# Optimization experiments

Measured on AMD Instinct MI355X. Metric: run time of the kernel, lower is better.

Reference implementation:

```python
import jax, jax.numpy as jnp
import numpy as np

B, L, D, M, R, W = 4, 2048, 2048, 64, 128, 4
SCALE = 1.0 / float(np.sqrt(M))
NORM_EPS = 1e-12


def setup_inputs() -> dict:
    key = jax.random.key(0)
    ks = jax.random.split(key, 8)
    s = lambda k, shape: jax.random.normal(k, shape, jnp.float32) * 0.02
    return dict(
        hidden_states=jax.random.normal(ks[0], (B, L, D), jnp.float32),
        conv_w=s(ks[1], (D, W)),                 # depthwise conv kernel (squeezed [D,1,W])
        conv_b=jnp.zeros((D,), jnp.float32),
        in_proj_w=s(ks[2], (2 * M, D)),          # r,k projection
        ch_gate_w0=s(ks[3], (R, D)),             # low-rank channel gate
        ch_gate_w1=s(ks[4], (D, R)),
        ch_gate_b1=jnp.zeros((D,), jnp.float32),
        mem_gate_w=s(ks[5], (2 * M, D)),         # select/tau gates
        mem_gate_b=jax.random.normal(ks[6], (2 * M,), jnp.float32),
        residual_weight=jnp.ones((D,), jnp.float32),
    )


def _causal_depthwise_conv(x, w, b):
    # x: [B,L,D], w: [D,W], b: [D]; y[t] = sum_i x[t-(W-1)+i] * w[:, i] + b
    xp = jnp.pad(x, ((0, 0), (W - 1, 0), (0, 0)))
    y = sum(xp[:, i:i + x.shape[1], :] * w[:, i] for i in range(W)) + b
    return jax.nn.silu(y)


def reference(hidden_states, conv_w, conv_b, in_proj_w, ch_gate_w0, ch_gate_w1,
              ch_gate_b1, mem_gate_w, mem_gate_b, residual_weight):
    x = hidden_states
    shift = _causal_depthwise_conv(x, conv_w, conv_b)          # [B,L,D]
    residual = shift

    rk = shift @ in_proj_w.T                                   # [B,L,2M]
    r, k = rk[..., :M], rk[..., M:]

    ch = jax.nn.sigmoid((x @ ch_gate_w0.T) @ ch_gate_w1.T + ch_gate_b1)
    u = ch * x                                                 # [B,L,D] gated value

    mg = shift @ mem_gate_w.T + mem_gate_b                     # [B,L,2M]
    sel = jax.nn.softplus(mg[..., :M])
    tau = jax.nn.sigmoid(mg[..., M:])
    it_gate = sel ** tau                                       # input gate
    g = -sel * tau                                             # log decay (rt_gate_log)

    # F.normalize(k) then scale by input gate
    k = k / jnp.maximum(jnp.linalg.norm(k, axis=-1, keepdims=True), NORM_EPS)
    k = k * it_gate

    # GLA recurrence: S_t = diag(exp(g_t)) S_{t-1} + k_t^T u_t; o_t = scale * r_t S_t
    def step(S, inp):
        r_t, k_t, u_t, g_t = inp                               # [B,M],[B,M],[B,D],[B,M]
        S = jnp.exp(g_t)[..., None] * S + k_t[..., None] * u_t[:, None, :]
        o_t = SCALE * jnp.einsum('bm,bmd->bd', r_t, S)
        return S, o_t

    xs = (jnp.swapaxes(r, 0, 1), jnp.swapaxes(k, 0, 1),
          jnp.swapaxes(u, 0, 1), jnp.swapaxes(g, 0, 1))
    S0 = jnp.zeros((x.shape[0], M, D), jnp.float32)
    _, o = jax.lax.scan(step, S0, xs)                          # o: [L,B,D]
    o = jnp.swapaxes(o, 0, 1)

    return o + residual * residual_weight
```

## Files before the change

kernel.cpp:

```cpp
#include <hip/hip_runtime.h>
#include <hip/hip_bf16.h>
#include <math.h>

#define B_ 4
#define L_ 2048
#define D_ 2048
#define M_ 64
#define R_ 128
#define NTOK (B_*L_)
#define SCALE_ 0.125f
#define C_ 32
#define NCH (L_/C_)

typedef __attribute__((ext_vector_type(8))) short short8;
typedef __attribute__((ext_vector_type(4))) float f32x4;

#define BAR() asm volatile("s_waitcnt lgkmcnt(0)\n\ts_barrier" ::: "memory")

#define MFMA(a, b, c) __builtin_amdgcn_mfma_f32_16x16x32_bf16((a), (b), (c), 0, 0, 0)

__device__ __forceinline__ unsigned short f2bfu(float v) {
    union { float f; unsigned u; } a; a.f = v;
    unsigned r = a.u + 0x7fffu + ((a.u >> 16) & 1u);
    return (unsigned short)(r >> 16);
}
__device__ __forceinline__ float bfu2f(unsigned short h) {
    union { unsigned u; float f; } a; a.u = ((unsigned)h) << 16;
    return a.f;
}
__device__ __forceinline__ unsigned pkbf(float a, float b) {
    union { __hip_bfloat162 h; unsigned u; } cv;
    cv.h = __float22bfloat162_rn(make_float2(a, b));
    return cv.u;
}

__global__ __launch_bounds__(256) void k_conv(const float* __restrict__ x,
    const float* __restrict__ cw, const float* __restrict__ cb,
    float* __restrict__ shift, unsigned short* __restrict__ sbf,
    unsigned short* __restrict__ xb)
{
    size_t i4 = (size_t)blockIdx.x * 256 + threadIdx.x;
    int dq = (int)(i4 % (D_ / 4));
    size_t n = i4 / (D_ / 4);
    int l = (int)(n % L_);
    int d0 = dq * 4;
    const float* xp = x + n * D_ + d0;
    float4 w0 = *(const float4*)(cw + (size_t)d0 * 4);
    float4 w1 = *(const float4*)(cw + (size_t)(d0 + 1) * 4);
    float4 w2 = *(const float4*)(cw + (size_t)(d0 + 2) * 4);
    float4 w3 = *(const float4*)(cw + (size_t)(d0 + 3) * 4);
    float4 acc = *(const float4*)(cb + d0);
    float4 xv3 = *(const float4*)xp;
#pragma unroll
    for (int i = 0; i < 3; i++) {
        if (l - 3 + i >= 0) {
            float4 xv = *(const float4*)(xp + (size_t)(i - 3) * D_);
            acc.x = fmaf(xv.x, ((const float*)&w0)[i], acc.x);
            acc.y = fmaf(xv.y, ((const float*)&w1)[i], acc.y);
            acc.z = fmaf(xv.z, ((const float*)&w2)[i], acc.z);
            acc.w = fmaf(xv.w, ((const float*)&w3)[i], acc.w);
        }
    }
    acc.x = fmaf(xv3.x, ((const float*)&w0)[3], acc.x);
    acc.y = fmaf(xv3.y, ((const float*)&w1)[3], acc.y);
    acc.z = fmaf(xv3.z, ((const float*)&w2)[3], acc.z);
    acc.w = fmaf(xv3.w, ((const float*)&w3)[3], acc.w);
    float4 o;
    o.x = acc.x / (1.f + expf(-acc.x));
    o.y = acc.y / (1.f + expf(-acc.y));
    o.z = acc.z / (1.f + expf(-acc.z));
    o.w = acc.w / (1.f + expf(-acc.w));
    *(float4*)(shift + n * D_ + d0) = o;
    uint2 sp; sp.x = pkbf(o.x, o.y); sp.y = pkbf(o.z, o.w);
    *(uint2*)(sbf + n * D_ + d0) = sp;
    uint2 xpk; xpk.x = pkbf(xv3.x, xv3.y); xpk.y = pkbf(xv3.z, xv3.w);
    *(uint2*)(xb + n * D_ + d0) = xpk;
}

__global__ __launch_bounds__(256) void k_castw(
    const float* __restrict__ s0, const float* __restrict__ s1,
    const float* __restrict__ s2, const float* __restrict__ s3,
    unsigned short* __restrict__ d0, unsigned short* __restrict__ d1,
    unsigned short* __restrict__ d2, unsigned short* __restrict__ d3)
{
    int which = blockIdx.x >> 8;
    int idx = ((blockIdx.x & 255) * 256 + threadIdx.x) * 4;
    const float* s = which == 0 ? s0 : which == 1 ? s1 : which == 2 ? s2 : s3;
    unsigned short* d = which == 0 ? d0 : which == 1 ? d1 : which == 2 ? d2 : d3;
    float4 v = *(const float4*)(s + idx);
    uint2 o;
    o.x = pkbf(v.x, v.y);
    o.y = pkbf(v.z, v.w);
    *(uint2*)(d + idx) = o;
}

__global__ __launch_bounds__(256) void k_gemm12(
    const unsigned short* __restrict__ sbf, const unsigned short* __restrict__ xb,
    const unsigned short* __restrict__ Wcatb, const unsigned short* __restrict__ w0b,
    float* __restrict__ rkmg, unsigned short* __restrict__ t1b)
{
    __shared__ __align__(16) unsigned short As[2][128 * 32];
    __shared__ __align__(16) unsigned short Bs[2][128 * 32];
    int tid = threadIdx.x;
    int n0 = blockIdx.x * 128;
    int y = blockIdx.y;
    const unsigned short* A = (y < 2) ? sbf : xb;
    const unsigned short* Bp = (y == 0) ? Wcatb : (y == 1) ? (Wcatb + 128 * 2048) : w0b;
    int wave = tid >> 6, lane = tid & 63;
    int quad = lane >> 4, lcol = lane & 15;
    int wrow = (wave >> 1) * 64, wcol = (wave & 1) * 64;
    int r0 = tid >> 2;
    int sub = (tid & 3) * 8;
    const unsigned short* a0p = A + (size_t)(n0 + r0) * 2048 + sub;
    const unsigned short* a1p = A + (size_t)(n0 + r0 + 64) * 2048 + sub;
    const unsigned short* b0p = Bp + (size_t)r0 * 2048 + sub;
    const unsigned short* b1p = Bp + (size_t)(r0 + 64) * 2048 + sub;

    f32x4 acc[4][4];
#pragma unroll
    for (int i = 0; i < 4; i++)
#pragma unroll
        for (int j = 0; j < 4; j++) acc[i][j] = {0.f, 0.f, 0.f, 0.f};

    uint4 av0 = *(const uint4*)a0p, av1 = *(const uint4*)a1p;
    uint4 bv0 = *(const uint4*)b0p, bv1 = *(const uint4*)b1p;
    {
        int i0 = tid * 8, i1 = 2048 + tid * 8;
        *(uint4*)&As[0][i0] = av0; *(uint4*)&As[0][i1] = av1;
        *(uint4*)&Bs[0][i0] = bv0; *(uint4*)&Bs[0][i1] = bv1;
    }
    av0 = *(const uint4*)(a0p + 32); av1 = *(const uint4*)(a1p + 32);
    bv0 = *(const uint4*)(b0p + 32); bv1 = *(const uint4*)(b1p + 32);
    BAR();

    for (int k32 = 0; k32 < 64; k32++) {
        int cur = k32 & 1;
        short8 af[4], bfr[4];
#pragma unroll
        for (int i = 0; i < 4; i++)
            af[i] = *(short8*)&As[cur][(wrow + i * 16 + lcol) * 32 + quad * 8];
#pragma unroll
        for (int j = 0; j < 4; j++)
            bfr[j] = *(short8*)&Bs[cur][(wcol + j * 16 + lcol) * 32 + quad * 8];
#pragma unroll
        for (int i = 0; i < 4; i++)
#pragma unroll
            for (int j = 0; j < 4; j++)
                acc[i][j] = MFMA(af[i], bfr[j], acc[i][j]);
        if (k32 + 1 < 64) {
            int nb = cur ^ 1;
            int i0 = tid * 8, i1 = 2048 + tid * 8;
            *(uint4*)&As[nb][i0] = av0; *(uint4*)&As[nb][i1] = av1;
            *(uint4*)&Bs[nb][i0] = bv0; *(uint4*)&Bs[nb][i1] = bv1;
        }
        if (k32 + 2 < 64) {
            int k0 = (k32 + 2) * 32;
            av0 = *(const uint4*)(a0p + k0); av1 = *(const uint4*)(a1p + k0);
            bv0 = *(const uint4*)(b0p + k0); bv1 = *(const uint4*)(b1p + k0);
        }
        BAR();
    }

#pragma unroll
    for (int i = 0; i < 4; i++)
#pragma unroll
        for (int j = 0; j < 4; j++)
#pragma unroll
            for (int q = 0; q < 4; q++) {
                int row = wrow + i * 16 + quad * 4 + q;
                int col = wcol + j * 16 + lcol;
                int n = n0 + row;
                if (y < 2) rkmg[(size_t)n * 256 + y * 128 + col] = acc[i][j][q];
                else       t1b[(size_t)n * 128 + col] = f2bfu(acc[i][j][q]);
            }
}

__global__ __launch_bounds__(256) void k_gemm3(
    const unsigned short* __restrict__ t1b, const unsigned short* __restrict__ w1b,
    const float* __restrict__ b1, const float* __restrict__ x,
    float* __restrict__ u)
{
    __shared__ __align__(16) unsigned short As[2][128 * 32];
    __shared__ __align__(16) unsigned short Bs[2][128 * 32];
    int tid = threadIdx.x;
    int n0 = blockIdx.x * 128;
    int jblk = blockIdx.y * 128;
    int wave = tid >> 6, lane = tid & 63;
    int quad = lane >> 4, lcol = lane & 15;
    int wrow = (wave >> 1) * 64, wcol = (wave & 1) * 64;
    int r0 = tid >> 2;
    int sub = (tid & 3) * 8;
    const unsigned short* a0p = t1b + (size_t)(n0 + r0) * 128 + sub;
    const unsigned short* a1p = t1b + (size_t)(n0 + r0 + 64) * 128 + sub;
    const unsigned short* b0p = w1b + (size_t)(jblk + r0) * 128 + sub;
    const unsigned short* b1p = w1b + (size_t)(jblk + r0 + 64) * 128 + sub;

    f32x4 acc[4][4];
#pragma unroll
    for (int i = 0; i < 4; i++)
#pragma unroll
        for (int j = 0; j < 4; j++) acc[i][j] = {0.f, 0.f, 0.f, 0.f};

    uint4 av0 = *(const uint4*)a0p, av1 = *(const uint4*)a1p;
    uint4 bv0 = *(const uint4*)b0p, bv1 = *(const uint4*)b1p;
    {
        int i0 = tid * 8, i1 = 2048 + tid * 8;
        *(uint4*)&As[0][i0] = av0; *(uint4*)&As[0][i1] = av1;
        *(uint4*)&Bs[0][i0] = bv0; *(uint4*)&Bs[0][i1] = bv1;
    }
    av0 = *(const uint4*)(a0p + 32); av1 = *(const uint4*)(a1p + 32);
    bv0 = *(const uint4*)(b0p + 32); bv1 = *(const uint4*)(b1p + 32);
    BAR();

    for (int k32 = 0; k32 < 4; k32++) {
        int cur = k32 & 1;
        short8 af[4], bfr[4];
#pragma unroll
        for (int i = 0; i < 4; i++)
            af[i] = *(short8*)&As[cur][(wrow + i * 16 + lcol) * 32 + quad * 8];
#pragma unroll
        for (int j = 0; j < 4; j++)
            bfr[j] = *(short8*)&Bs[cur][(wcol + j * 16 + lcol) * 32 + quad * 8];
#pragma unroll
        for (int i = 0; i < 4; i++)
#pragma unroll
            for (int j = 0; j < 4; j++)
                acc[i][j] = MFMA(af[i], bfr[j], acc[i][j]);
        if (k32 + 1 < 4) {
            int nb = cur ^ 1;
            int i0 = tid * 8, i1 = 2048 + tid * 8;
            *(uint4*)&As[nb][i0] = av0; *(uint4*)&As[nb][i1] = av1;
            *(uint4*)&Bs[nb][i0] = bv0; *(uint4*)&Bs[nb][i1] = bv1;
        }
        if (k32 + 2 < 4) {
            int k0 = (k32 + 2) * 32;
            av0 = *(const uint4*)(a0p + k0); av1 = *(const uint4*)(a1p + k0);
            bv0 = *(const uint4*)(b0p + k0); bv1 = *(const uint4*)(b1p + k0);
        }
        BAR();
    }

#pragma unroll
    for (int i = 0; i < 4; i++)
#pragma unroll
        for (int j = 0; j < 4; j++)
#pragma unroll
            for (int q = 0; q < 4; q++) {
                int row = wrow + i * 16 + quad * 4 + q;
                int col = wcol + j * 16 + lcol;
                int n = n0 + row, jc = jblk + col;
                float val = acc[i][j][q] + b1[jc];
                val = 1.f / (1.f + expf(-val));
                val *= x[(size_t)n * D_ + jc];
                u[(size_t)n * D_ + jc] = val;
            }
}

__global__ __launch_bounds__(256) void k_prep(const float* __restrict__ rkmg,
    const float* __restrict__ mb,
    unsigned short* __restrict__ Rt, unsigned short* __restrict__ Kc,
    float* __restrict__ Ac, unsigned short* __restrict__ Pg)
{
    __shared__ float seg[4 * 64];
    __shared__ __align__(16) unsigned short rtL[32 * 72];
    __shared__ __align__(16) unsigned short kdL[32 * 72];
    int blk = blockIdx.x;
    int sg = threadIdx.x >> 6, mm = threadIdx.x & 63;
    int n0 = blk * C_ + sg * 8;

    float rr[8], kk[8], lamr[8];
    float csum = 0.f;
#pragma unroll
    for (int j = 0; j < 8; j++) {
        const float* row = rkmg + (size_t)(n0 + j) * 256;
        float r   = row[mm];
        float k   = row[64 + mm];
        float mg1 = row[128 + mm] + mb[mm];
        float mg2 = row[192 + mm] + mb[64 + mm];
        float sel = (mg1 > 20.f) ? mg1 : log1pf(expf(mg1));
        float tau = 1.f / (1.f + expf(-mg2));
        float it  = expf(tau * logf(sel));
        float g   = -sel * tau;
        float s2  = k * k;
#pragma unroll
        for (int off = 32; off >= 1; off >>= 1) s2 += __shfl_xor(s2, off, 64);
        float kn = k / fmaxf(sqrtf(s2), 1e-12f);
        rr[j] = r;
        kk[j] = kn * it;
        csum += g;
        lamr[j] = csum;
    }
    seg[sg * 64 + mm] = csum;
    __syncthreads();
    float off = 0.f, tot = 0.f;
#pragma unroll
    for (int s = 0; s < 4; s++) {
        float v = seg[s * 64 + mm];
        if (s < sg) off += v;
        tot += v;
    }
    size_t obase = (size_t)blk * (C_ * 64);
    unsigned short kcp[8];
#pragma unroll
    for (int j = 0; j < 8; j++) {
        float lam = off + lamr[j];
        unsigned short rv = f2bfu(rr[j] * expf(lam));
        unsigned short kv = f2bfu(kk[j] * expf(-lam));
        int t = sg * 8 + j;
        Rt[obase + (size_t)t * 64 + mm] = rv;
        rtL[t * 72 + mm] = rv;
        kdL[t * 72 + mm] = kv;
        kcp[j] = f2bfu(kk[j] * expf(tot - lam));
    }
    ushort4 ka4, kb4;
    ka4.x = kcp[0]; ka4.y = kcp[1]; ka4.z = kcp[2]; ka4.w = kcp[3];
    kb4.x = kcp[4]; kb4.y = kcp[5]; kb4.z = kcp[6]; kb4.w = kcp[7];
    *(ushort4*)&Kc[obase + (size_t)mm * C_ + sg * 8]     = ka4;
    *(ushort4*)&Kc[obase + (size_t)mm * C_ + sg * 8 + 4] = kb4;
    if (sg == 0) Ac[(size_t)blk * 64 + mm] = expf(tot);
    __syncthreads();

    int lane = threadIdx.x & 63, quad = lane >> 4, l15 = lane & 15;
    size_t pb = (size_t)blk * 1024;
    if (sg < 3) {
        int ti = (sg == 0) ? 0 : 16;
        int si = (sg == 2) ? 16 : 0;
        short8 a0 = *(const short8*)&rtL[(ti + l15) * 72 + quad * 8];
        short8 a1 = *(const short8*)&rtL[(ti + l15) * 72 + 32 + quad * 8];
        short8 b0 = *(const short8*)&kdL[(si + l15) * 72 + quad * 8];
        short8 b1 = *(const short8*)&kdL[(si + l15) * 72 + 32 + quad * 8];
        f32x4 pp = {0.f, 0.f, 0.f, 0.f};
        pp = MFMA(a0, b0, pp);
        pp = MFMA(a1, b1, pp);
#pragma unroll
        for (int q = 0; q < 4; q++) {
            int t = ti + quad * 4 + q, s = si + l15;
            Pg[pb + t * 32 + s] = f2bfu((s <= t) ? pp[q] : 0.f);
        }
    } else {
#pragma unroll
        for (int q = 0; q < 4; q++)
            Pg[pb + (quad * 4 + q) * 32 + 16 + l15] = 0;
    }
}

#define STAGE(q) do { \
    int t_ = tid >> 3, m8_ = (tid & 7) * 8; \
    *(uint4*)&rtS[q][t_ * 72 + m8_] = rtv; \
    int m_ = tid >> 2, s8_ = (tid & 3) * 8; \
    *(uint4*)&kcS[q][m_ * 40 + s8_] = kcv; \
    int s4_ = (tid & 7) * 4; \
    *(ushort4*)&PlS[q][t_ * 40 + s4_] = plv; \
    int dd_ = tid & 31, tt_ = tid >> 5; \
    _Pragma("unroll") \
    for (int j_ = 0; j_ < 4; j_++) { \
        unsigned short h_ = f2bfu(uv[j_]); \
        UTh[q][dd_ * 40 + tt_ + 8 * j_] = h_; \
        UTl[q][dd_ * 40 + tt_ + 8 * j_] = f2bfu(uv[j_] - bfu2f(h_)); \
    } \
    if (tid < 64) aCs[q][tid] = acv; \
} while (0)

#define PREFETCH(n) do { \
    size_t g_ = cbase + (size_t)(n) * 2048 + (size_t)tid * 8; \
    rtv = *(const uint4*)(Rt + g_); \
    kcv = *(const uint4*)(Kc + g_); \
    plv = *(const ushort4*)(Pg + pbase + (size_t)(n) * 1024 + tid * 4); \
    size_t un_ = ubase + (size_t)(n) * C_ * D_; \
    int dd_ = tid & 31, tt_ = tid >> 5; \
    _Pragma("unroll") \
    for (int j_ = 0; j_ < 4; j_++) \
        uv[j_] = u[un_ + (size_t)(tt_ + 8 * j_) * D_ + dd_]; \
    if (tid < 64) acv = Ac[(size_t)(bNCH + (n)) * 64 + tid]; \
} while (0)

__global__ __launch_bounds__(256) void k_chunk(
    const unsigned short* __restrict__ Rt, const unsigned short* __restrict__ Kc,
    const float* __restrict__ Ac, const unsigned short* __restrict__ Pg,
    const float* __restrict__ u, const float* __restrict__ shift,
    const float* __restrict__ rw, float* __restrict__ out)
{
    __shared__ __align__(16) unsigned short rtS[2][32 * 72];
    __shared__ __align__(16) unsigned short PlS[2][32 * 40];
    __shared__ __align__(16) unsigned short kcS[2][64 * 40];
    __shared__ __align__(16) unsigned short UTh[2][32 * 40];
    __shared__ __align__(16) unsigned short UTl[2][32 * 40];
    __shared__ __align__(16) unsigned short STh[2][32 * 72];
    __shared__ __align__(16) unsigned short STl[2][32 * 72];
    __shared__ float aCs[2][64];

    int tid = threadIdx.x;
    int wave = tid >> 6, lane = tid & 63;
    int quad = lane >> 4, l15 = lane & 15;
    int b = blockIdx.x & 3, slice = blockIdx.x >> 2;
    int d0 = slice * 32;
    int bNCH = b * NCH;

    for (int i = tid; i < 2 * 32 * 72; i += 256) {
        (&STh[0][0])[i] = 0; (&STl[0][0])[i] = 0;
    }

    size_t cbase = (size_t)b * (L_ * 64);
    size_t pbase = (size_t)bNCH * 1024;
    size_t ubase = (size_t)b * L_ * D_ + d0;

    float rwv = (wave < 2) ? rw[d0 + wave * 16 + l15] : 0.f;

    uint4 rtv, kcv;
    ushort4 plv;
    float uv[4], acv = 0.f;
    float sv[8], svn[8];
    size_t sadr = ubase + (size_t)wave * 16 + l15 + (size_t)(quad * 4) * D_;

    PREFETCH(0);
    STAGE(0);
    PREFETCH(1);
    if (wave < 2) {
#pragma unroll
        for (int tile = 0; tile < 2; tile++)
#pragma unroll
            for (int q = 0; q < 4; q++)
                sv[tile * 4 + q] = shift[sadr + (size_t)(tile * 16 + q) * D_];
    }
    BAR();

    f32x4 zz = {0.f, 0.f, 0.f, 0.f};
    f32x4 sreg[4];
#pragma unroll
    for (int mt = 0; mt < 4; mt++) sreg[mt] = zz;

    for (int c = 0; c < NCH; c++) {
        int p = c & 1;
        if (c + 1 < NCH) STAGE(p ^ 1);
        if (c + 2 < NCH) PREFETCH(c + 2);

        if (wave < 2) {
            if (c + 1 < NCH) {
                size_t s0_ = sadr + (size_t)(c + 1) * C_ * D_;
#pragma unroll
                for (int tile = 0; tile < 2; tile++)
#pragma unroll
                    for (int q = 0; q < 4; q++)
                        svn[tile * 4 + q] = shift[s0_ + (size_t)(tile * 16 + q) * D_];
            }
            int h = wave;
            short8 a00 = *(const short8*)&rtS[p][l15 * 72 + quad * 8];
            short8 a01 = *(const short8*)&rtS[p][l15 * 72 + 32 + quad * 8];
            short8 a10 = *(const short8*)&rtS[p][(16 + l15) * 72 + quad * 8];
            short8 a11 = *(const short8*)&rtS[p][(16 + l15) * 72 + 32 + quad * 8];
            const unsigned short* sbh = &STh[p ^ 1][(h * 16 + l15) * 72];
            const unsigned short* sbl = &STl[p ^ 1][(h * 16 + l15) * 72];
            short8 sh0 = *(const short8*)&sbh[quad * 8];
            short8 sh1 = *(const short8*)&sbh[32 + quad * 8];
            short8 sl0 = *(const short8*)&sbl[quad * 8];
            short8 sl1 = *(const short8*)&sbl[32 + quad * 8];
            short8 pa0 = *(const short8*)&PlS[p][l15 * 40 + quad * 8];
            short8 pa1 = *(const short8*)&PlS[p][(16 + l15) * 40 + quad * 8];
            short8 uh = *(const short8*)&UTh[p][(h * 16 + l15) * 40 + quad * 8];
            short8 ul = *(const short8*)&UTl[p][(h * 16 + l15) * 40 + quad * 8];
            __builtin_amdgcn_s_setprio(1);
            f32x4 oA0 = MFMA(a00, sh0, zz); oA0 = MFMA(a01, sh1, oA0); oA0 = MFMA(pa0, uh, oA0);
            f32x4 oB0 = MFMA(a00, sl0, zz); oB0 = MFMA(a01, sl1, oB0); oB0 = MFMA(pa0, ul, oB0);
            f32x4 oA1 = MFMA(a10, sh0, zz); oA1 = MFMA(a11, sh1, oA1); oA1 = MFMA(pa1, uh, oA1);
            f32x4 oB1 = MFMA(a10, sl0, zz); oB1 = MFMA(a11, sl1, oB1); oB1 = MFMA(pa1, ul, oB1);
            __builtin_amdgcn_s_setprio(0);
            size_t oa = ubase + (size_t)(c * C_ + quad * 4) * D_ + h * 16 + l15;
#pragma unroll
            for (int q = 0; q < 4; q++) {
                out[oa + (size_t)q * D_]        = SCALE_ * (oA0[q] + oB0[q]) + sv[q] * rwv;
                out[oa + (size_t)(16 + q) * D_] = SCALE_ * (oA1[q] + oB1[q]) + sv[4 + q] * rwv;
            }
#pragma unroll
            for (int q = 0; q < 8; q++) sv[q] = svn[q];
        } else {
            int h = wave - 2;
            short8 uh = *(const short8*)&UTh[p][(h * 16 + l15) * 40 + quad * 8];
            short8 ul = *(const short8*)&UTl[p][(h * 16 + l15) * 40 + quad * 8];
            __builtin_amdgcn_s_setprio(1);
#pragma unroll
            for (int mt = 0; mt < 4; mt++) {
                f32x4 a4 = *(const f32x4*)&aCs[p][mt * 16 + quad * 4];
                f32x4 s = sreg[mt];
                s[0] *= a4[0]; s[1] *= a4[1]; s[2] *= a4[2]; s[3] *= a4[3];
                short8 ka = *(const short8*)&kcS[p][(mt * 16 + l15) * 40 + quad * 8];
                s = MFMA(ka, uh, s);
                s = MFMA(ka, ul, s);
                sreg[mt] = s;
                unsigned hA = pkbf(s[0], s[1]);
                unsigned hB = pkbf(s[2], s[3]);
                float f0 = bfu2f((unsigned short)hA), f1 = bfu2f((unsigned short)(hA >> 16));
                float f2 = bfu2f((unsigned short)hB), f3 = bfu2f((unsigned short)(hB >> 16));
                unsigned lA = pkbf(s[0] - f0, s[1] - f1);
                unsigned lB = pkbf(s[2] - f2, s[3] - f3);
                int sidx = (h * 16 + l15) * 72 + mt * 16 + quad * 4;
                uint2 wh; wh.x = hA; wh.y = hB;
                uint2 wl; wl.x = lA; wl.y = lB;
                *(uint2*)&STh[p][sidx] = wh;
                *(uint2*)&STl[p][sidx] = wl;
            }
            __builtin_amdgcn_s_setprio(0);
        }
        BAR();
    }
}

extern "C" void kernel_launch(void* const* d_in, const int* in_sizes, int n_in,
                              void* d_out, int out_size, void* d_ws, size_t ws_size,
                              hipStream_t stream)
{
    const float* x   = (const float*)d_in[0];
    const float* cw  = (const float*)d_in[1];
    const float* cb  = (const float*)d_in[2];
    const float* ipw = (const float*)d_in[3];
    const float* w0  = (const float*)d_in[4];
    const float* w1  = (const float*)d_in[5];
    const float* b1  = (const float*)d_in[6];
    const float* mw  = (const float*)d_in[7];
    const float* mb  = (const float*)d_in[8];
    const float* rw  = (const float*)d_in[9];
    float* out = (float*)d_out;

    float* ws    = (float*)d_ws;
    float* shift = ws;
    float* u     = shift + (size_t)NTOK * D_;
    unsigned short* xb  = (unsigned short*)u;
    unsigned short* sbf = xb + (size_t)NTOK * D_;
    float* rkmg = u + (size_t)NTOK * D_;
    float* Ac   = rkmg + (size_t)NTOK * 256;
    unsigned short* Rt  = (unsigned short*)(Ac + (size_t)B_ * NCH * 64);
    unsigned short* Kc  = Rt + (size_t)NTOK * 64;
    unsigned short* Pg  = Kc + (size_t)NTOK * 64;
    unsigned short* t1b = Pg + (size_t)B_ * NCH * 1024;
    unsigned short* Wcatb = t1b + (size_t)NTOK * 128;
    unsigned short* w0b   = Wcatb + 256 * 2048;
    unsigned short* w1b   = w0b + 128 * 2048;

    k_conv<<<(NTOK * (size_t)D_) / 1024, 256, 0, stream>>>(x, cw, cb, shift, sbf, xb);

    k_castw<<<1024, 256, 0, stream>>>(ipw, mw, w0, w1,
                                      Wcatb, Wcatb + 128 * 2048, w0b, w1b);

    k_gemm12<<<dim3(64, 3), 256, 0, stream>>>(sbf, xb, Wcatb, w0b, rkmg, t1b);

    k_prep<<<B_ * NCH, 256, 0, stream>>>(rkmg, mb, Rt, Kc, Ac, Pg);

    k_gemm3<<<dim3(64, 16), 256, 0, stream>>>(t1b, w1b, b1, x, u);

    k_chunk<<<256, 256, 0, stream>>>(Rt, Kc, Ac, Pg, u, shift, rw, out);
}
```

Measured before the change: 325.5 us.

## Store shift as bf16 hi/lo pair, register-block conv, retile gemm12 for occupancy

The conv kernel now computes 8 consecutive tokens per thread, reusing the loaded input rows from registers instead of reloading the 3 halo rows for every token. It drops the fp32 shift buffer and writes a bf16 high/low split, which the chunk kernel recombines for the residual, and the high part doubles as the GEMM operand. gemm12 moves from 128x128 tiles (192 blocks) to 64x64 tiles with padded LDS rows (768 blocks) to fill more CUs and reduce bank conflicts. The risk is lower arithmetic intensity per block in gemm12, and the residual is now held to roughly 16-bit mantissa precision.

```diff
diff --git a/kernel.cpp b/kernel.cpp
--- a/kernel.cpp
+++ b/kernel.cpp
@@ -36,45 +36,60 @@
 
 __global__ __launch_bounds__(256) void k_conv(const float* __restrict__ x,
     const float* __restrict__ cw, const float* __restrict__ cb,
-    float* __restrict__ shift, unsigned short* __restrict__ sbf,
+    unsigned short* __restrict__ sh, unsigned short* __restrict__ sl,
     unsigned short* __restrict__ xb)
 {
-    size_t i4 = (size_t)blockIdx.x * 256 + threadIdx.x;
-    int dq = (int)(i4 % (D_ / 4));
-    size_t n = i4 / (D_ / 4);
-    int l = (int)(n % L_);
+    size_t gid = (size_t)blockIdx.x * 256 + threadIdx.x;
+    int dq = (int)(gid & 511);
+    size_t tg = gid >> 9;
     int d0 = dq * 4;
-    const float* xp = x + n * D_ + d0;
+    size_t n0 = tg * 8;
+    int l0 = (int)(n0 & (L_ - 1));
+    const float* xp = x + n0 * D_ + d0;
     float4 w0 = *(const float4*)(cw + (size_t)d0 * 4);
     float4 w1 = *(const float4*)(cw + (size_t)(d0 + 1) * 4);
     float4 w2 = *(const float4*)(cw + (size_t)(d0 + 2) * 4);
     float4 w3 = *(const float4*)(cw + (size_t)(d0 + 3) * 4);
-    float4 acc = *(const float4*)(cb + d0);
-    float4 xv3 = *(const float4*)xp;
-#pragma unroll
-    for (int i = 0; i < 3; i++) {
-        if (l - 3 + i >= 0) {
-            float4 xv = *(const float4*)(xp + (size_t)(i - 3) * D_);
+    float4 bias = *(const float4*)(cb + d0);
+    float4 v[11];
+    if (l0 > 0) {
+        v[0] = *(const float4*)(xp - 3 * D_);
+        v[1] = *(const float4*)(xp - 2 * D_);
+        v[2] = *(const float4*)(xp - 1 * D_);
+    } else {
+        v[0] = make_float4(0.f, 0.f, 0.f, 0.f);
+        v[1] = v[0]; v[2] = v[0];
+    }
+#pragma unroll
+    for (int j = 0; j < 8; j++) v[3 + j] = *(const float4*)(xp + (size_t)j * D_);
+#pragma unroll
+    for (int j = 0; j < 8; j++) {
+        float4 acc = bias;
+#pragma unroll
+        for (int i = 0; i < 4; i++) {
+            float4 xv = v[j + i];
             acc.x = fmaf(xv.x, ((const float*)&w0)[i], acc.x);
             acc.y = fmaf(xv.y, ((const float*)&w1)[i], acc.y);
             acc.z = fmaf(xv.z, ((const float*)&w2)[i], acc.z);
             acc.w = fmaf(xv.w, ((const float*)&w3)[i], acc.w);
         }
-    }
-    acc.x = fmaf(xv3.x, ((const float*)&w0)[3], acc.x);
-    acc.y = fmaf(xv3.y, ((const float*)&w1)[3], acc.y);
-    acc.z = fmaf(xv3.z, ((const float*)&w2)[3], acc.z);
-    acc.w = fmaf(xv3.w, ((const float*)&w3)[3], acc.w);
-    float4 o;
-    o.x = acc.x / (1.f + expf(-acc.x));
-    o.y = acc.y / (1.f + expf(-acc.y));
-    o.z = acc.z / (1.f + expf(-acc.z));
-    o.w = acc.w / (1.f + expf(-acc.w));
-    *(float4*)(shift + n * D_ + d0) = o;
-    uint2 sp; sp.x = pkbf(o.x, o.y); sp.y = pkbf(o.z, o.w);
-    *(uint2*)(sbf + n * D_ + d0) = sp;
-    uint2 xpk; xpk.x = pkbf(xv3.x, xv3.y); xpk.y = pkbf(xv3.z, xv3.w);
-    *(uint2*)(xb + n * D_ + d0) = xpk;
+        float4 o;
+        o.x = acc.x / (1.f + expf(-acc.x));
+        o.y = acc.y / (1.f + expf(-acc.y));
+        o.z = acc.z / (1.f + expf(-acc.z));
+        o.w = acc.w / (1.f + expf(-acc.w));
+        ushort4 hv, lv;
+        hv.x = f2bfu(o.x); lv.x = f2bfu(o.x - bfu2f(hv.x));
+        hv.y = f2bfu(o.y); lv.y = f2bfu(o.y - bfu2f(hv.y));
+        hv.z = f2bfu(o.z); lv.z = f2bfu(o.z - bfu2f(hv.z));
+        hv.w = f2bfu(o.w); lv.w = f2bfu(o.w - bfu2f(hv.w));
+        size_t oo = (n0 + j) * D_ + d0;
+        *(ushort4*)(sh + oo) = hv;
+        *(ushort4*)(sl + oo) = lv;
+        float4 xv = v[3 + j];
+        uint2 xpk; xpk.x = pkbf(xv.x, xv.y); xpk.y = pkbf(xv.z, xv.w);
+        *(uint2*)(xb + oo) = xpk;
+    }
 }
 
 __global__ __launch_bounds__(256) void k_castw(
@@ -99,79 +114,74 @@
     const unsigned short* __restrict__ Wcatb, const unsigned short* __restrict__ w0b,
     float* __restrict__ rkmg, unsigned short* __restrict__ t1b)
 {
-    __shared__ __align__(16) unsigned short As[2][128 * 32];
-    __shared__ __align__(16) unsigned short Bs[2][128 * 32];
+    __shared__ __align__(16) unsigned short As[2][64 * 72];
+    __shared__ __align__(16) unsigned short Bs[2][64 * 72];
     int tid = threadIdx.x;
-    int n0 = blockIdx.x * 128;
-    int y = blockIdx.y;
-    const unsigned short* A = (y < 2) ? sbf : xb;
-    const unsigned short* Bp = (y == 0) ? Wcatb : (y == 1) ? (Wcatb + 128 * 2048) : w0b;
+    int y = blockIdx.x;
+    int n0 = blockIdx.y * 64;
+    const unsigned short* A = (y < 4) ? sbf : xb;
+    const unsigned short* Bp = (y < 4) ? (Wcatb + (size_t)y * 64 * 2048)
+                                       : (w0b + (size_t)(y - 4) * 64 * 2048);
     int wave = tid >> 6, lane = tid & 63;
     int quad = lane >> 4, lcol = lane & 15;
-    int wrow = (wave >> 1) * 64, wcol = (wave & 1) * 64;
-    int r0 = tid >> 2;
-    int sub = (tid & 3) * 8;
-    const unsigned short* a0p = A + (size_t)(n0 + r0) * 2048 + sub;
-    const unsigned short* a1p = A + (size_t)(n0 + r0 + 64) * 2048 + sub;
-    const unsigned short* b0p = Bp + (size_t)r0 * 2048 + sub;
-    const unsigned short* b1p = Bp + (size_t)(r0 + 64) * 2048 + sub;
-
-    f32x4 acc[4][4];
-#pragma unroll
-    for (int i = 0; i < 4; i++)
-#pragma unroll
-        for (int j = 0; j < 4; j++) acc[i][j] = {0.f, 0.f, 0.f, 0.f};
-
-    uint4 av0 = *(const uint4*)a0p, av1 = *(const uint4*)a1p;
-    uint4 bv0 = *(const uint4*)b0p, bv1 = *(const uint4*)b1p;
-    {
-        int i0 = tid * 8, i1 = 2048 + tid * 8;
-        *(uint4*)&As[0][i0] = av0; *(uint4*)&As[0][i1] = av1;
-        *(uint4*)&Bs[0][i0] = bv0; *(uint4*)&Bs[0][i1] = bv1;
-    }
-    av0 = *(const uint4*)(a0p + 32); av1 = *(const uint4*)(a1p + 32);
-    bv0 = *(const uint4*)(b0p + 32); bv1 = *(const uint4*)(b1p + 32);
+    int wrow = (wave >> 1) * 32, wcol = (wave & 1) * 32;
+    int r0 = tid >> 2, sub = (tid & 3) * 8;
+    const unsigned short* ap = A + (size_t)(n0 + r0) * 2048 + sub;
+    const unsigned short* bp = Bp + (size_t)r0 * 2048 + sub;
+    int sidx = r0 * 72 + sub;
+
+    f32x4 acc[2][2];
+#pragma unroll
+    for (int i = 0; i < 2; i++)
+#pragma unroll
+        for (int j = 0; j < 2; j++) acc[i][j] = {0.f, 0.f, 0.f, 0.f};
+
+    uint4 av = *(const uint4*)ap;
+    uint4 bv = *(const uint4*)bp;
+    *(uint4*)&As[0][sidx] = av;
+    *(uint4*)&Bs[0][sidx] = bv;
+    av = *(const uint4*)(ap + 32);
+    bv = *(const uint4*)(bp + 32);
     BAR();
 
     for (int k32 = 0; k32 < 64; k32++) {
         int cur = k32 & 1;
-        short8 af[4], bfr[4];
-#pragma unroll
-        for (int i = 0; i < 4; i++)
-            af[i] = *(short8*)&As[cur][(wrow + i * 16 + lcol) * 32 + quad * 8];
-#pragma unroll
-        for (int j = 0; j < 4; j++)
-            bfr[j] = *(short8*)&Bs[cur][(wcol + j * 16 + lcol) * 32 + quad * 8];
-#pragma unroll
-        for (int i = 0; i < 4; i++)
-#pragma unroll
-            for (int j = 0; j < 4; j++)
+        short8 af[2], bfr[2];
+#pragma unroll
+        for (int i = 0; i < 2; i++)
+            af[i] = *(short8*)&As[cur][(wrow + i * 16 + lcol) * 72 + quad * 8];
+#pragma unroll
+        for (int j = 0; j < 2; j++)
+            bfr[j] = *(short8*)&Bs[cur][(wcol + j * 16 + lcol) * 72 + quad * 8];
+#pragma unroll
+        for (int i = 0; i < 2; i++)
+#pragma unroll
+            for (int j = 0; j < 2; j++)
                 acc[i][j] = MFMA(af[i], bfr[j], acc[i][j]);
         if (k32 + 1 < 64) {
             int nb = cur ^ 1;
-            int i0 = tid * 8, i1 = 2048 + tid * 8;
-            *(uint4*)&As[nb][i0] = av0; *(uint4*)&As[nb][i1] = av1;
-            *(uint4*)&Bs[nb][i0] = bv0; *(uint4*)&Bs[nb][i1] = bv1;
+            *(uint4*)&As[nb][sidx] = av;
+            *(uint4*)&Bs[nb][sidx] = bv;
         }
         if (k32 + 2 < 64) {
             int k0 = (k32 + 2) * 32;
-            av0 = *(const uint4*)(a0p + k0); av1 = *(const uint4*)(a1p + k0);
-            bv0 = *(const uint4*)(b0p + k0); bv1 = *(const uint4*)(b1p + k0);
+            av = *(const uint4*)(ap + k0);
+            bv = *(const uint4*)(bp + k0);
         }
         BAR();
     }
 
 #pragma unroll
-    for (int i = 0; i < 4; i++)
-#pragma unroll
-        for (int j = 0; j < 4; j++)
+    for (int i = 0; i < 2; i++)
+#pragma unroll
+        for (int j = 0; j < 2; j++)
 #pragma unroll
             for (int q = 0; q < 4; q++) {
                 int row = wrow + i * 16 + quad * 4 + q;
                 int col = wcol + j * 16 + lcol;
                 int n = n0 + row;
-                if (y < 2) rkmg[(size_t)n * 256 + y * 128 + col] = acc[i][j][q];
-                else       t1b[(size_t)n * 128 + col] = f2bfu(acc[i][j][q]);
+                if (y < 4) rkmg[(size_t)n * 256 + y * 64 + col] = acc[i][j][q];
+                else       t1b[(size_t)n * 128 + (y - 4) * 64 + col] = f2bfu(acc[i][j][q]);
             }
 }
 
@@ -377,7 +387,8 @@
 __global__ __launch_bounds__(256) void k_chunk(
     const unsigned short* __restrict__ Rt, const unsigned short* __restrict__ Kc,
     const float* __restrict__ Ac, const unsigned short* __restrict__ Pg,
-    const float* __restrict__ u, const float* __restrict__ shift,
+    const float* __restrict__ u, const unsigned short* __restrict__ sh,
+    const unsigned short* __restrict__ sl,
     const float* __restrict__ rw, float* __restrict__ out)
 {
     __shared__ __align__(16) unsigned short rtS[2][32 * 72];
@@ -409,7 +420,7 @@
     uint4 rtv, kcv;
     ushort4 plv;
     float uv[4], acv = 0.f;
-    float sv[8], svn[8];
+    unsigned short svh[8], svl[8], svhn[8], svln[8];
     size_t sadr = ubase + (size_t)wave * 16 + l15 + (size_t)(quad * 4) * D_;
 
     PREFETCH(0);
@@ -419,8 +430,10 @@
 #pragma unroll
         for (int tile = 0; tile < 2; tile++)
 #pragma unroll
-            for (int q = 0; q < 4; q++)
-                sv[tile * 4 + q] = shift[sadr + (size_t)(tile * 16 + q) * D_];
+            for (int q = 0; q < 4; q++) {
+                svh[tile * 4 + q] = sh[sadr + (size_t)(tile * 16 + q) * D_];
+                svl[tile * 4 + q] = sl[sadr + (size_t)(tile * 16 + q) * D_];
+            }
     }
     BAR();
 
@@ -440,8 +453,10 @@
 #pragma unroll
                 for (int tile = 0; tile < 2; tile++)
 #pragma unroll
-                    for (int q = 0; q < 4; q++)
-                        svn[tile * 4 + q] = shift[s0_ + (size_t)(tile * 16 + q) * D_];
+                    for (int q = 0; q < 4; q++) {
+                        svhn[tile * 4 + q] = sh[s0_ + (size_t)(tile * 16 + q) * D_];
+                        svln[tile * 4 + q] = sl[s0_ + (size_t)(tile * 16 + q) * D_];
+                    }
             }
             int h = wave;
             short8 a00 = *(const short8*)&rtS[p][l15 * 72 + quad * 8];
@@ -467,11 +482,13 @@
             size_t oa = ubase + (size_t)(c * C_ + quad * 4) * D_ + h * 16 + l15;
 #pragma unroll
             for (int q = 0; q < 4; q++) {
-                out[oa + (size_t)q * D_]        = SCALE_ * (oA0[q] + oB0[q]) + sv[q] * rwv;
-                out[oa + (size_t)(16 + q) * D_] = SCALE_ * (oA1[q] + oB1[q]) + sv[4 + q] * rwv;
+                float r0v = bfu2f(svh[q]) + bfu2f(svl[q]);
+                float r1v = bfu2f(svh[4 + q]) + bfu2f(svl[4 + q]);
+                out[oa + (size_t)q * D_]        = SCALE_ * (oA0[q] + oB0[q]) + r0v * rwv;
+                out[oa + (size_t)(16 + q) * D_] = SCALE_ * (oA1[q] + oB1[q]) + r1v * rwv;
             }
 #pragma unroll
-            for (int q = 0; q < 8; q++) sv[q] = svn[q];
+            for (int q = 0; q < 8; q++) { svh[q] = svhn[q]; svl[q] = svln[q]; }
         } else {
             int h = wave - 2;
             short8 uh = *(const short8*)&UTh[p][(h * 16 + l15) * 40 + quad * 8];
@@ -520,11 +537,10 @@
     const float* rw  = (const float*)d_in[9];
     float* out = (float*)d_out;
 
-    float* ws    = (float*)d_ws;
-    float* shift = ws;
-    float* u     = shift + (size_t)NTOK * D_;
-    unsigned short* xb  = (unsigned short*)u;
-    unsigned short* sbf = xb + (size_t)NTOK * D_;
+    unsigned short* sh = (unsigned short*)d_ws;
+    unsigned short* sl = sh + (size_t)NTOK * D_;
+    unsigned short* xb = sl + (size_t)NTOK * D_;
+    float* u = (float*)xb;
     float* rkmg = u + (size_t)NTOK * D_;
     float* Ac   = rkmg + (size_t)NTOK * 256;
     unsigned short* Rt  = (unsigned short*)(Ac + (size_t)B_ * NCH * 64);
@@ -535,16 +551,16 @@
     unsigned short* w0b   = Wcatb + 256 * 2048;
     unsigned short* w1b   = w0b + 128 * 2048;
 
-    k_conv<<<(NTOK * (size_t)D_) / 1024, 256, 0, stream>>>(x, cw, cb, shift, sbf, xb);
+    k_conv<<<(NTOK / 8) * (D_ / 4) / 256, 256, 0, stream>>>(x, cw, cb, sh, sl, xb);
 
     k_castw<<<1024, 256, 0, stream>>>(ipw, mw, w0, w1,
                                       Wcatb, Wcatb + 128 * 2048, w0b, w1b);
 
-    k_gemm12<<<dim3(64, 3), 256, 0, stream>>>(sbf, xb, Wcatb, w0b, rkmg, t1b);
+    k_gemm12<<<dim3(6, 128), 256, 0, stream>>>(sh, xb, Wcatb, w0b, rkmg, t1b);
 
     k_prep<<<B_ * NCH, 256, 0, stream>>>(rkmg, mb, Rt, Kc, Ac, Pg);
 
     k_gemm3<<<dim3(64, 16), 256, 0, stream>>>(t1b, w1b, b1, x, u);
 
-    k_chunk<<<256, 256, 0, stream>>>(Rt, Kc, Ac, Pg, u, shift, rw, out);
-}
+    k_chunk<<<256, 256, 0, stream>>>(Rt, Kc, Ac, Pg, u, sh, sl, rw, out);
+}
```

Measured after the change: 284.7 us. -12.6%, faster.
